# Kernel optimization log

Measured on AMD Instinct MI355X. Metric: run time of the kernel, lower is better.

Reference implementation:

```python
import jax, jax.numpy as jnp
import numpy as np

N_NODES = 100000
N_EDGES = 1600000
D = 128
NEG_SLOPE = 0.01  # torch F.leaky_relu default


def setup_inputs() -> dict:
    key = jax.random.key(0)
    k1, k2, k3, k4, k5, k6 = jax.random.split(key, 6)
    input = jax.random.normal(k1, (N_NODES, D), dtype=jnp.float32)
    edge_row = jax.random.randint(k2, (N_EDGES,), 0, N_NODES, dtype=jnp.int32)
    edge_col = jax.random.randint(k3, (N_EDGES,), 0, N_NODES, dtype=jnp.int32)
    edge_val = jax.random.uniform(k4, (N_EDGES,), dtype=jnp.float32)
    # learned params: W1: Linear(D, D, bias=False), W2: Linear(2D, D, bias=False)
    # torch stores weight as [out, in]; apply as x @ W.T
    bound1 = 1.0 / np.sqrt(D)
    bound2 = 1.0 / np.sqrt(2 * D)
    W1 = jax.random.uniform(k5, (D, D), dtype=jnp.float32, minval=-bound1, maxval=bound1)
    W2 = jax.random.uniform(k6, (D, 2 * D), dtype=jnp.float32, minval=-bound2, maxval=bound2)
    return {"input": input, "edge_row": edge_row, "edge_col": edge_col,
            "edge_val": edge_val, "W1": W1, "W2": W2}


def reference(input, edge_row, edge_col, edge_val, W1, W2):
    # proj_input = W1(input)
    proj = input @ W1.T                                   # [N, D]
    # neighboor = spmm(adj, proj): out[i] = sum_e val[e] * proj[col[e]] for row[e]==i
    msg = edge_val[:, None] * proj[edge_col]              # [E, D]
    neigh = jax.ops.segment_sum(msg, edge_row, num_segments=input.shape[0])  # [N, D]
    h = jnp.concatenate([input + neigh, input * neigh], axis=-1)  # [N, 2D]
    return jax.nn.leaky_relu(h @ W2.T, NEG_SLOPE)         # [N, D]
```

## Files before the change

kernel.cpp:

```cpp
#include <hip/hip_runtime.h>

#define DIM 128
#define BROWS 128
#define BCAP 3072
#define NBUK_PAD 800
#define BK_EDGES 6144

typedef __attribute__((ext_vector_type(8))) short short8;
typedef __attribute__((ext_vector_type(4))) float f32x4;

__device__ __forceinline__ unsigned short f2bf(float f) {
    unsigned u = __float_as_uint(f);
    u += 0x7fffu + ((u >> 16) & 1u);
    return (unsigned short)(u >> 16);
}
__device__ __forceinline__ float bf2f(unsigned short b) {
    return __uint_as_float(((unsigned)b) << 16);
}

__global__ void k_pre(const float4* __restrict__ in, const float* __restrict__ W1,
                      const float* __restrict__ W2, unsigned short* __restrict__ inputb,
                      unsigned short* __restrict__ w1b, unsigned short* __restrict__ w2b,
                      int* __restrict__ gcur, int n4, int nCvt, int nbuk) {
    int b = blockIdx.x;
    if (b < nCvt) {
        int i = b * 256 + threadIdx.x;
        if (i < n4) {
            float4 v = in[i];
            *(ushort4*)(inputb + (long)i * 4) =
                make_ushort4(f2bf(v.x), f2bf(v.y), f2bf(v.z), f2bf(v.w));
        }
    } else if (b < nCvt + 192) {
        int idx = (b - nCvt) * 256 + threadIdx.x;
        if (idx < 16384)      w1b[idx] = f2bf(W1[idx]);
        else                  w2b[idx - 16384] = f2bf(W2[idx - 16384]);
    } else {
        int i = (b - nCvt - 192) * 256 + threadIdx.x;
        if (i < nbuk) gcur[i] = 0;
    }
}

__global__ __launch_bounds__(1024) void k_bucket(const int* __restrict__ er,
                                                 const int* __restrict__ ec,
                                                 const float* __restrict__ ev,
                                                 int* __restrict__ gcur,
                                                 int2* __restrict__ edata0, int E, int nbuk) {
    __shared__ int2 sed[BK_EDGES];
    __shared__ int lhist[NBUK_PAD];
    __shared__ int lscan[NBUK_PAD];
    __shared__ int lpos[NBUK_PAD];
    __shared__ int gbase[NBUK_PAD];
    int tid = threadIdx.x;
    if (tid < NBUK_PAD) lhist[tid] = 0;
    __syncthreads();
    int e0 = blockIdx.x * BK_EDGES;
    int bcnt = E - e0; if (bcnt > BK_EDGES) bcnt = BK_EDGES;
    for (int i = tid; i < bcnt; i += 1024)
        atomicAdd(&lhist[er[e0 + i] >> 7], 1);
    __syncthreads();
    if (tid < NBUK_PAD) lscan[tid] = lhist[tid];
    __syncthreads();
    for (int off = 1; off < NBUK_PAD; off <<= 1) {
        int v = (tid < NBUK_PAD && tid >= off) ? lscan[tid - off] : 0;
        __syncthreads();
        if (tid < NBUK_PAD) lscan[tid] += v;
        __syncthreads();
    }
    if (tid < NBUK_PAD) {
        int c = lhist[tid];
        lpos[tid] = lscan[tid] - c;
        gbase[tid] = (c > 0 && tid < nbuk) ? atomicAdd(&gcur[tid], c) : 0;
    }
    __syncthreads();
    for (int i = tid; i < bcnt; i += 1024) {
        int e = e0 + i;
        int r = er[e], bk = r >> 7;
        int p = atomicAdd(&lpos[bk], 1);
        sed[p] = make_int2(((r & 127) << 17) | ec[e], __float_as_int(ev[e]));
    }
    __syncthreads();
    int wv = tid >> 6, lane = tid & 63;
    for (int bk = wv; bk < nbuk; bk += 16) {
        int c = lhist[bk];
        if (c == 0) continue;
        int excl = lscan[bk] - c;
        int gb = gbase[bk];
        long base = (long)bk * BCAP;
        for (int j = lane; j < c; j += 64)
            if (gb + j < BCAP)
                edata0[base + gb + j] = sed[excl + j];
    }
}

__global__ __launch_bounds__(256) void k_gather(const unsigned short* __restrict__ xb,
                                                const int2* __restrict__ edata0,
                                                const int* __restrict__ gcur,
                                                unsigned short* __restrict__ aggb, int N) {
    __shared__ int2 sed[BCAP];
    __shared__ int hist[BROWS];
    __shared__ int hscan[BROWS];
    __shared__ int lcur[BROWS];
    int tid = threadIdx.x, b = blockIdx.x;
    int cnt = gcur[b]; if (cnt > BCAP) cnt = BCAP;
    const int2* e0 = edata0 + (long)b * BCAP;
    if (tid < BROWS) hist[tid] = 0;
    __syncthreads();
    for (int i = tid; i < cnt; i += 256) atomicAdd(&hist[e0[i].x >> 17], 1);
    __syncthreads();
    if (tid < BROWS) hscan[tid] = hist[tid];
    __syncthreads();
    for (int off = 1; off < BROWS; off <<= 1) {
        int v = (tid < BROWS && tid >= off) ? hscan[tid - off] : 0;
        __syncthreads();
        if (tid < BROWS) hscan[tid] += v;
        __syncthreads();
    }
    if (tid < BROWS) lcur[tid] = hscan[tid] - hist[tid];
    __syncthreads();
    for (int i = tid; i < cnt; i += 256) {
        int2 v = e0[i];
        int p = atomicAdd(&lcur[v.x >> 17], 1);
        sed[p] = make_int2(v.x & 0x1FFFF, v.y);
    }
    __syncthreads();

    int slot = tid >> 4, s = tid & 15;
    const int4* x4 = (const int4*)xb;

#define ACC8(U, V)                                                         \
    {                                                                      \
        const unsigned* wp_ = (const unsigned*)&(U);                       \
        pa[0] += (V) * __uint_as_float(wp_[0] << 16);                      \
        pa[1] += (V) * __uint_as_float(wp_[0] & 0xffff0000u);              \
        pa[2] += (V) * __uint_as_float(wp_[1] << 16);                      \
        pa[3] += (V) * __uint_as_float(wp_[1] & 0xffff0000u);              \
        pa[4] += (V) * __uint_as_float(wp_[2] << 16);                      \
        pa[5] += (V) * __uint_as_float(wp_[2] & 0xffff0000u);              \
        pa[6] += (V) * __uint_as_float(wp_[3] << 16);                      \
        pa[7] += (V) * __uint_as_float(wp_[3] & 0xffff0000u);              \
    }

    for (int k = 0; k < 8; ++k) {
        int rl = k * 16 + slot;
        int row = b * BROWS + rl;
        int beg = hscan[rl] - hist[rl], end = hscan[rl];
        float pa[8];
#pragma unroll
        for (int t = 0; t < 8; ++t) pa[t] = 0.f;
        int j = beg;
        for (; j + 4 <= end; j += 4) {
            int2 q0 = sed[j], q1 = sed[j + 1], q2 = sed[j + 2], q3 = sed[j + 3];
            int4 u0 = x4[(long)q0.x * 16 + s];
            int4 u1 = x4[(long)q1.x * 16 + s];
            int4 u2 = x4[(long)q2.x * 16 + s];
            int4 u3 = x4[(long)q3.x * 16 + s];
            float v0 = __int_as_float(q0.y), v1 = __int_as_float(q1.y);
            float v2 = __int_as_float(q2.y), v3 = __int_as_float(q3.y);
            ACC8(u0, v0);
            ACC8(u1, v1);
            ACC8(u2, v2);
            ACC8(u3, v3);
        }
        for (; j < end; ++j) {
            int2 q = sed[j];
            int4 u = x4[(long)q.x * 16 + s];
            float v = __int_as_float(q.y);
            ACC8(u, v);
        }
        if (row < N) {
            short8 o;
#pragma unroll
            for (int t = 0; t < 8; ++t) o[t] = (short)f2bf(pa[t]);
            *(short8*)(aggb + (long)row * DIM + s * 8) = o;
        }
    }
#undef ACC8
}

__global__ __launch_bounds__(256, 4) void k_fused(const unsigned short* __restrict__ aggb,
                                                  const unsigned short* __restrict__ inputb,
                                                  const unsigned short* __restrict__ w1b,
                                                  const unsigned short* __restrict__ w2b,
                                                  float* __restrict__ out, int N) {
    __shared__ __align__(16) unsigned short sh[2 * 64 * 136];
    int w = threadIdx.x >> 6, lane = threadIdx.x & 63;
    int quad = lane >> 4, lq = lane & 15;
    int blk0 = blockIdx.x * 64;
    unsigned short* sh0 = sh;
    unsigned short* sh1 = sh + 64 * 136;

    short8 b1[2][4];
#pragma unroll
    for (int ntl = 0; ntl < 2; ++ntl)
#pragma unroll
        for (int kb = 0; kb < 4; ++kb)
            b1[ntl][kb] = *(const short8*)(w1b + ((w * 2 + ntl) * 16 + lq) * DIM +
                                           kb * 32 + quad * 8);

#pragma unroll
    for (int mt = 0; mt < 4; ++mt) {
        short8 afr[4];
        {
            int row = blk0 + mt * 16 + lq; if (row >= N) row = N - 1;
#pragma unroll
            for (int kb = 0; kb < 4; ++kb)
                afr[kb] = *(const short8*)(aggb + (long)row * DIM + kb * 32 + quad * 8);
        }
#pragma unroll
        for (int ntl = 0; ntl < 2; ++ntl) {
            f32x4 c = {0.f, 0.f, 0.f, 0.f};
#pragma unroll
            for (int kb = 0; kb < 4; ++kb)
                c = __builtin_amdgcn_mfma_f32_16x16x32_bf16(afr[kb], b1[ntl][kb], c, 0, 0, 0);
            int nt = w * 2 + ntl;
#pragma unroll
            for (int rg = 0; rg < 4; ++rg) {
                int r = blk0 + mt * 16 + quad * 4 + rg;
                int rr = (r < N) ? r : (N - 1);
                float x = bf2f(inputb[(long)rr * DIM + nt * 16 + lq]);
                float nb = c[rg];
                int off = (mt * 16 + quad * 4 + rg) * 136 + nt * 16 + lq;
                sh0[off] = f2bf(x + nb);
                sh1[off] = f2bf(x * nb);
            }
        }
    }

    short8 b2[2][8];
#pragma unroll
    for (int ntl = 0; ntl < 2; ++ntl)
#pragma unroll
        for (int kb = 0; kb < 8; ++kb)
            b2[ntl][kb] = *(const short8*)(w2b + ((w * 2 + ntl) * 16 + lq) * 256 +
                                           kb * 32 + quad * 8);
    __syncthreads();

#pragma unroll
    for (int mt = 0; mt < 4; ++mt) {
        int arow = (mt * 16 + lq) * 136;
        short8 a0[4], a1[4];
#pragma unroll
        for (int kb = 0; kb < 4; ++kb) {
            a0[kb] = *(const short8*)(sh0 + arow + kb * 32 + quad * 8);
            a1[kb] = *(const short8*)(sh1 + arow + kb * 32 + quad * 8);
        }
#pragma unroll
        for (int ntl = 0; ntl < 2; ++ntl) {
            f32x4 c = {0.f, 0.f, 0.f, 0.f};
#pragma unroll
            for (int kb = 0; kb < 4; ++kb)
                c = __builtin_amdgcn_mfma_f32_16x16x32_bf16(a0[kb], b2[ntl][kb], c, 0, 0, 0);
#pragma unroll
            for (int kb = 0; kb < 4; ++kb)
                c = __builtin_amdgcn_mfma_f32_16x16x32_bf16(a1[kb], b2[ntl][kb + 4], c, 0, 0, 0);
            int nt = w * 2 + ntl;
#pragma unroll
            for (int rg = 0; rg < 4; ++rg) {
                int r = blk0 + mt * 16 + quad * 4 + rg;
                if (r < N) {
                    float v = c[rg];
                    v = (v > 0.f) ? v : 0.01f * v;
                    out[(long)r * DIM + nt * 16 + lq] = v;
                }
            }
        }
    }
}

extern "C" void kernel_launch(void* const* d_in, const int* in_sizes, int n_in,
                              void* d_out, int out_size, void* d_ws, size_t ws_size,
                              hipStream_t stream) {
    const float* input = (const float*)d_in[0];
    const int*   er    = (const int*)d_in[1];
    const int*   ec    = (const int*)d_in[2];
    const float* ev    = (const float*)d_in[3];
    const float* W1    = (const float*)d_in[4];
    const float* W2    = (const float*)d_in[5];
    int N = in_sizes[0] / DIM;
    int E = in_sizes[1];
    float* out = (float*)d_out;
    int nbuk = (N + BROWS - 1) / BROWS;

    int* ws = (int*)d_ws;
    int* gcur = ws;
    int2* edata0 = (int2*)(ws + 1024);
    unsigned short* w1b = (unsigned short*)(edata0 + (long)nbuk * BCAP);
    unsigned short* w2b = w1b + 16384;
    unsigned short* inputb = w2b + 32768;
    unsigned short* aggb = inputb + (long)N * DIM;

    int n4 = N * (DIM / 4);
    int nCvt = (n4 + 255) / 256;
    int nZero = (nbuk + 255) / 256;
    k_pre<<<nCvt + 192 + nZero, 256, 0, stream>>>(
        (const float4*)input, W1, W2, inputb, w1b, w2b, gcur, n4, nCvt, nbuk);

    k_bucket<<<(E + BK_EDGES - 1) / BK_EDGES, 1024, 0, stream>>>(
        er, ec, ev, gcur, edata0, E, nbuk);

    k_gather<<<nbuk, 256, 0, stream>>>(inputb, edata0, gcur, aggb, N);

    k_fused<<<(N + 63) / 64, 256, 0, stream>>>(aggb, inputb, w1b, w2b, out, N);
}
```

Baseline: 249.8 us.

## Merge conversion into bucketing kernel, widen gather blocks, stage input tile in LDS

Merges the input/weight bf16 conversion and the edge bucketing into one launch, with a tiny separate kernel zeroing the bucket counters first. This removes a kernel boundary and lets the conversion blocks overlap with bucketing. The bucket write-out now assigns 8 lanes per bucket instead of a whole wavefront. The gather kernel moves to 512 threads with 32 row slots. The fused GEMM kernel stages the 64x128 input tile in shared memory with coalesced loads instead of scattered 2-byte global reads, at the cost of lowering the occupancy hint to 3 blocks.

```diff
diff --git a/kernel.cpp b/kernel.cpp
--- a/kernel.cpp
+++ b/kernel.cpp
@@ -18,81 +18,85 @@
     return __uint_as_float(((unsigned)b) << 16);
 }
 
-__global__ void k_pre(const float4* __restrict__ in, const float* __restrict__ W1,
-                      const float* __restrict__ W2, unsigned short* __restrict__ inputb,
-                      unsigned short* __restrict__ w1b, unsigned short* __restrict__ w2b,
-                      int* __restrict__ gcur, int n4, int nCvt, int nbuk) {
-    int b = blockIdx.x;
-    if (b < nCvt) {
-        int i = b * 256 + threadIdx.x;
-        if (i < n4) {
-            float4 v = in[i];
-            *(ushort4*)(inputb + (long)i * 4) =
-                make_ushort4(f2bf(v.x), f2bf(v.y), f2bf(v.z), f2bf(v.w));
-        }
-    } else if (b < nCvt + 192) {
-        int idx = (b - nCvt) * 256 + threadIdx.x;
-        if (idx < 16384)      w1b[idx] = f2bf(W1[idx]);
-        else                  w2b[idx - 16384] = f2bf(W2[idx - 16384]);
-    } else {
-        int i = (b - nCvt - 192) * 256 + threadIdx.x;
-        if (i < nbuk) gcur[i] = 0;
-    }
-}
-
-__global__ __launch_bounds__(1024) void k_bucket(const int* __restrict__ er,
-                                                 const int* __restrict__ ec,
-                                                 const float* __restrict__ ev,
-                                                 int* __restrict__ gcur,
-                                                 int2* __restrict__ edata0, int E, int nbuk) {
+__global__ void k_zero(int* __restrict__ gcur, int nbuk) {
+    int i = threadIdx.x;
+    if (i < nbuk) gcur[i] = 0;
+}
+
+__global__ __launch_bounds__(1024) void k_prep(const float4* __restrict__ in,
+                                               const float* __restrict__ W1,
+                                               const float* __restrict__ W2,
+                                               const int* __restrict__ er,
+                                               const int* __restrict__ ec,
+                                               const float* __restrict__ ev,
+                                               int* __restrict__ gcur,
+                                               int2* __restrict__ edata0,
+                                               unsigned short* __restrict__ inputb,
+                                               unsigned short* __restrict__ w1b,
+                                               unsigned short* __restrict__ w2b,
+                                               int E, int nbuk, int nBkt, int n4) {
     __shared__ int2 sed[BK_EDGES];
     __shared__ int lhist[NBUK_PAD];
     __shared__ int lscan[NBUK_PAD];
     __shared__ int lpos[NBUK_PAD];
     __shared__ int gbase[NBUK_PAD];
-    int tid = threadIdx.x;
-    if (tid < NBUK_PAD) lhist[tid] = 0;
-    __syncthreads();
-    int e0 = blockIdx.x * BK_EDGES;
-    int bcnt = E - e0; if (bcnt > BK_EDGES) bcnt = BK_EDGES;
-    for (int i = tid; i < bcnt; i += 1024)
-        atomicAdd(&lhist[er[e0 + i] >> 7], 1);
-    __syncthreads();
-    if (tid < NBUK_PAD) lscan[tid] = lhist[tid];
-    __syncthreads();
-    for (int off = 1; off < NBUK_PAD; off <<= 1) {
-        int v = (tid < NBUK_PAD && tid >= off) ? lscan[tid - off] : 0;
-        __syncthreads();
-        if (tid < NBUK_PAD) lscan[tid] += v;
-        __syncthreads();
-    }
-    if (tid < NBUK_PAD) {
-        int c = lhist[tid];
-        lpos[tid] = lscan[tid] - c;
-        gbase[tid] = (c > 0 && tid < nbuk) ? atomicAdd(&gcur[tid], c) : 0;
-    }
-    __syncthreads();
-    for (int i = tid; i < bcnt; i += 1024) {
-        int e = e0 + i;
-        int r = er[e], bk = r >> 7;
-        int p = atomicAdd(&lpos[bk], 1);
-        sed[p] = make_int2(((r & 127) << 17) | ec[e], __float_as_int(ev[e]));
-    }
-    __syncthreads();
-    int wv = tid >> 6, lane = tid & 63;
-    for (int bk = wv; bk < nbuk; bk += 16) {
-        int c = lhist[bk];
-        if (c == 0) continue;
-        int excl = lscan[bk] - c;
-        int gb = gbase[bk];
-        long base = (long)bk * BCAP;
-        for (int j = lane; j < c; j += 64)
-            if (gb + j < BCAP)
-                edata0[base + gb + j] = sed[excl + j];
-    }
-}
-
-__global__ __launch_bounds__(256) void k_gather(const unsigned short* __restrict__ xb,
+    int b = blockIdx.x, tid = threadIdx.x;
+
+    if (b < nBkt) {
+        if (tid < NBUK_PAD) lhist[tid] = 0;
+        __syncthreads();
+        int e0 = b * BK_EDGES;
+        int bcnt = E - e0; if (bcnt > BK_EDGES) bcnt = BK_EDGES;
+        for (int i = tid; i < bcnt; i += 1024)
+            atomicAdd(&lhist[er[e0 + i] >> 7], 1);
+        __syncthreads();
+        if (tid < NBUK_PAD) lscan[tid] = lhist[tid];
+        __syncthreads();
+        for (int off = 1; off < NBUK_PAD; off <<= 1) {
+            int v = (tid < NBUK_PAD && tid >= off) ? lscan[tid - off] : 0;
+            __syncthreads();
+            if (tid < NBUK_PAD) lscan[tid] += v;
+            __syncthreads();
+        }
+        if (tid < NBUK_PAD) {
+            int c = lhist[tid];
+            lpos[tid] = lscan[tid] - c;
+            gbase[tid] = (c > 0 && tid < nbuk) ? atomicAdd(&gcur[tid], c) : 0;
+        }
+        __syncthreads();
+        for (int i = tid; i < bcnt; i += 1024) {
+            int e = e0 + i;
+            int r = er[e], bk = r >> 7;
+            int p = atomicAdd(&lpos[bk], 1);
+            sed[p] = make_int2(((r & 127) << 17) | ec[e], __float_as_int(ev[e]));
+        }
+        __syncthreads();
+        int sub = tid & 7, bg = tid >> 3;
+        for (int bk = bg; bk < nbuk; bk += 128) {
+            int c = lhist[bk];
+            if (c == 0) continue;
+            int excl = lscan[bk] - c;
+            int gb = gbase[bk];
+            long base = (long)bk * BCAP;
+            for (int j = sub; j < c; j += 8)
+                if (gb + j < BCAP)
+                    edata0[base + gb + j] = sed[excl + j];
+        }
+    } else if (b < nBkt + 48) {
+        int idx = (b - nBkt) * 1024 + tid;
+        if (idx < 16384)      w1b[idx] = f2bf(W1[idx]);
+        else                  w2b[idx - 16384] = f2bf(W2[idx - 16384]);
+    } else {
+        int i = (b - nBkt - 48) * 1024 + tid;
+        if (i < n4) {
+            float4 v = in[i];
+            *(ushort4*)(inputb + (long)i * 4) =
+                make_ushort4(f2bf(v.x), f2bf(v.y), f2bf(v.z), f2bf(v.w));
+        }
+    }
+}
+
+__global__ __launch_bounds__(512) void k_gather(const unsigned short* __restrict__ xb,
                                                 const int2* __restrict__ edata0,
                                                 const int* __restrict__ gcur,
                                                 unsigned short* __restrict__ aggb, int N) {
@@ -105,7 +109,7 @@
     const int2* e0 = edata0 + (long)b * BCAP;
     if (tid < BROWS) hist[tid] = 0;
     __syncthreads();
-    for (int i = tid; i < cnt; i += 256) atomicAdd(&hist[e0[i].x >> 17], 1);
+    for (int i = tid; i < cnt; i += 512) atomicAdd(&hist[e0[i].x >> 17], 1);
     __syncthreads();
     if (tid < BROWS) hscan[tid] = hist[tid];
     __syncthreads();
@@ -117,7 +121,7 @@
     }
     if (tid < BROWS) lcur[tid] = hscan[tid] - hist[tid];
     __syncthreads();
-    for (int i = tid; i < cnt; i += 256) {
+    for (int i = tid; i < cnt; i += 512) {
         int2 v = e0[i];
         int p = atomicAdd(&lcur[v.x >> 17], 1);
         sed[p] = make_int2(v.x & 0x1FFFF, v.y);
@@ -140,8 +144,8 @@
         pa[7] += (V) * __uint_as_float(wp_[3] & 0xffff0000u);              \
     }
 
-    for (int k = 0; k < 8; ++k) {
-        int rl = k * 16 + slot;
+    for (int k = 0; k < 4; ++k) {
+        int rl = k * 32 + slot;
         int row = b * BROWS + rl;
         int beg = hscan[rl] - hist[rl], end = hscan[rl];
         float pa[8];
@@ -177,18 +181,26 @@
 #undef ACC8
 }
 
-__global__ __launch_bounds__(256, 4) void k_fused(const unsigned short* __restrict__ aggb,
+__global__ __launch_bounds__(256, 3) void k_fused(const unsigned short* __restrict__ aggb,
                                                   const unsigned short* __restrict__ inputb,
                                                   const unsigned short* __restrict__ w1b,
                                                   const unsigned short* __restrict__ w2b,
                                                   float* __restrict__ out, int N) {
     __shared__ __align__(16) unsigned short sh[2 * 64 * 136];
+    __shared__ __align__(16) unsigned short xs[64 * 136];
     int w = threadIdx.x >> 6, lane = threadIdx.x & 63;
     int quad = lane >> 4, lq = lane & 15;
     int blk0 = blockIdx.x * 64;
     unsigned short* sh0 = sh;
     unsigned short* sh1 = sh + 64 * 136;
 
+    for (int i = threadIdx.x; i < 64 * 16; i += 256) {
+        int row = i >> 4, c = i & 15;
+        int rr = blk0 + row; if (rr >= N) rr = N - 1;
+        *(short8*)(xs + row * 136 + c * 8) =
+            *(const short8*)(inputb + (long)rr * DIM + c * 8);
+    }
+
     short8 b1[2][4];
 #pragma unroll
     for (int ntl = 0; ntl < 2; ++ntl)
@@ -196,6 +208,7 @@
         for (int kb = 0; kb < 4; ++kb)
             b1[ntl][kb] = *(const short8*)(w1b + ((w * 2 + ntl) * 16 + lq) * DIM +
                                            kb * 32 + quad * 8);
+    __syncthreads();
 
 #pragma unroll
     for (int mt = 0; mt < 4; ++mt) {
@@ -215,11 +228,10 @@
             int nt = w * 2 + ntl;
 #pragma unroll
             for (int rg = 0; rg < 4; ++rg) {
-                int r = blk0 + mt * 16 + quad * 4 + rg;
-                int rr = (r < N) ? r : (N - 1);
-                float x = bf2f(inputb[(long)rr * DIM + nt * 16 + lq]);
+                int lrow = mt * 16 + quad * 4 + rg;
+                float x = bf2f(xs[lrow * 136 + nt * 16 + lq]);
                 float nb = c[rg];
-                int off = (mt * 16 + quad * 4 + rg) * 136 + nt * 16 + lq;
+                int off = lrow * 136 + nt * 16 + lq;
                 sh0[off] = f2bf(x + nb);
                 sh1[off] = f2bf(x * nb);
             }
@@ -290,15 +302,16 @@
     unsigned short* aggb = inputb + (long)N * DIM;
 
     int n4 = N * (DIM / 4);
-    int nCvt = (n4 + 255) / 256;
-    int nZero = (nbuk + 255) / 256;
-    k_pre<<<nCvt + 192 + nZero, 256, 0, stream>>>(
-        (const float4*)input, W1, W2, inputb, w1b, w2b, gcur, n4, nCvt, nbuk);
-
-    k_bucket<<<(E + BK_EDGES - 1) / BK_EDGES, 1024, 0, stream>>>(
-        er, ec, ev, gcur, edata0, E, nbuk);
-
-    k_gather<<<nbuk, 256, 0, stream>>>(inputb, edata0, gcur, aggb, N);
+    int nBkt = (E + BK_EDGES - 1) / BK_EDGES;
+    int nCvt = (n4 + 1023) / 1024;
+
+    k_zero<<<1, 1024, 0, stream>>>(gcur, nbuk);
+
+    k_prep<<<nBkt + 48 + nCvt, 1024, 0, stream>>>(
+        (const float4*)input, W1, W2, er, ec, ev, gcur, edata0,
+        inputb, w1b, w2b, E, nbuk, nBkt, n4);
+
+    k_gather<<<nbuk, 512, 0, stream>>>(inputb, edata0, gcur, aggb, N);
 
     k_fused<<<(N + 63) / 64, 256, 0, stream>>>(aggb, inputb, w1b, w2b, out, N);
 }
```

Measured after the change: 233.9 us. 6.3% less time.
